# Kernel optimization log

Measured on AMD Instinct MI355X. Metric: run time of the kernel, lower is better.

The kernel has to match this reference:

```python
import jax, jax.numpy as jnp
import numpy as np

DELTA_T = 0.25
K_SUB = int(round(1.0 / DELTA_T))  # Euler substeps per observation (unit-spaced times)


def setup_inputs() -> dict:
    key = jax.random.key(0)
    ks = jax.random.split(key, 16)
    B, T, IN, XH, G, HID, OUT = 512, 128, 128, 512, 256, 256, 128
    s = 0.05
    inp = {
        "H": jax.random.normal(ks[0], (B, T, IN), jnp.float32),
        "times": jnp.arange(T, dtype=jnp.int64 if jax.config.jax_enable_x64 else jnp.int32).reshape(1, T),
        # x_model: Linear(IN,XH) -> ReLU -> Linear(XH,G); stored as [in,out]
        "W1": jax.random.normal(ks[1], (IN, XH), jnp.float32) * s,
        "b1": jax.random.normal(ks[2], (XH,), jnp.float32) * s,
        "W2": jax.random.normal(ks[3], (XH, G), jnp.float32) * s,
        "b2": jax.random.normal(ks[4], (G,), jnp.float32) * s,
        # FullGRUODECell_Autonomous: three bias-free [HID,HID] linears (torch [out,in])
        "Ohr": jax.random.normal(ks[5], (HID, HID), jnp.float32) * s,
        "Ohz": jax.random.normal(ks[6], (HID, HID), jnp.float32) * s,
        "Ohh": jax.random.normal(ks[7], (HID, HID), jnp.float32) * s,
        # torch.nn.GRU(G, HID): weights [3H, in], gate order r,z,n
        "Wih": jax.random.normal(ks[8], (3 * HID, G), jnp.float32) * s,
        "Whh": jax.random.normal(ks[9], (3 * HID, HID), jnp.float32) * s,
        "bih": jax.random.normal(ks[10], (3 * HID,), jnp.float32) * s,
        "bhh": jax.random.normal(ks[11], (3 * HID,), jnp.float32) * s,
        # rec_linear: Linear(G, OUT), stored as [in,out]
        "Wr": jax.random.normal(ks[12], (G, OUT), jnp.float32) * s,
        "br": jax.random.normal(ks[13], (OUT,), jnp.float32) * s,
    }
    return inp


def _forward(H, W1, b1, W2, b2, Ohr, Ohz, Ohh, Wih, Whh, bih, bhh, Wr, br):
    # x_model
    HH = jnp.maximum(H @ W1 + b1, 0.0) @ W2 + b2  # [B, T, G]
    B = HH.shape[0]
    HID = Ohr.shape[0]

    # GRU-ODE Euler substep (autonomous cell: input is implicitly zero)
    def ode_substep(h, _):
        r = jax.nn.sigmoid(h @ Ohr.T)
        z = jax.nn.sigmoid(h @ Ohz.T)
        u = jnp.tanh((r * h) @ Ohh.T)
        return h + DELTA_T * ((1.0 - z) * (u - h)), None

    Wir, Wiz, Win = jnp.split(Wih, 3, axis=0)
    Uhr, Uhz, Uhn = jnp.split(Whh, 3, axis=0)
    bir, biz, bin_ = jnp.split(bih, 3)
    bhr, bhz, bhn = jnp.split(bhh, 3)

    def step(h, x_t):  # x_t: [B, G]
        h, _ = jax.lax.scan(ode_substep, h, None, length=K_SUB)
        r = jax.nn.sigmoid(x_t @ Wir.T + bir + h @ Uhr.T + bhr)
        z = jax.nn.sigmoid(x_t @ Wiz.T + biz + h @ Uhz.T + bhz)
        n = jnp.tanh(x_t @ Win.T + bin_ + r * (h @ Uhn.T + bhn))
        h_new = (1.0 - z) * n + z * h  # GRU output for one step == new hidden
        return h_new, h_new

    h0 = jnp.zeros((B, HID), HH.dtype)
    _, outs = jax.lax.scan(step, h0, jnp.swapaxes(HH, 0, 1))  # [T, B, HID]
    out = jnp.swapaxes(outs, 0, 1)  # [B, T, HID] (== gru_input_size)
    return out @ Wr + br  # identity last activation


def reference(H, times, W1, b1, W2, b2, Ohr, Ohz, Ohh, Wih, Whh, bih, bhh, Wr, br):
    # times are unit-spaced (arange); the data-dependent while-loop of the
    # original reduces to exactly K_SUB Euler substeps before each observation.
    return _forward(H, W1, b1, W2, b2, Ohr, Ohz, Ohh, Wih, Whh, bih, bhh, Wr, br)
```

## Files before the change

### kernel.cpp

```cpp
#include <hip/hip_runtime.h>

typedef unsigned short ushort;
typedef unsigned int uint;
typedef __bf16 bf16x8 __attribute__((ext_vector_type(8)));
typedef ushort ushort8 __attribute__((ext_vector_type(8)));
typedef float f32x4 __attribute__((ext_vector_type(4)));

#define Z4 f32x4{0.f, 0.f, 0.f, 0.f}

__device__ __forceinline__ f32x4 mfma16(bf16x8 a, bf16x8 b, f32x4 c) {
    return __builtin_amdgcn_mfma_f32_16x16x32_bf16(a, b, c, 0, 0, 0);
}
__device__ __forceinline__ float bf2f(ushort h) {
    union { uint u; float f; } v; v.u = ((uint)h) << 16; return v.f;
}
__device__ __forceinline__ ushort f2bf(float f) {
    union { float f; uint u; } v; v.f = f;
    uint u = v.u;
    uint r = (u + 0x7fffu + ((u >> 16) & 1u)) >> 16;
    return (ushort)r;
}
__device__ __forceinline__ float sigmoidf_(float x) { return 1.f / (1.f + __expf(-x)); }
__device__ __forceinline__ float tanhf_(float x) {
    float e = __expf(2.f * x);
    return 1.f - 2.f / (e + 1.f);
}

typedef __attribute__((address_space(1))) uint guint;
typedef __attribute__((address_space(3))) uint luint;
__device__ __forceinline__ void dma16(const ushort* g, ushort* l) {
    __builtin_amdgcn_global_load_lds((const guint*)g, (luint*)l, 16, 0, 0);
}
template <int N> __device__ __forceinline__ void ring_wait() {
    asm volatile("s_waitcnt vmcnt(%0)" ::"n"(N) : "memory");
}
__device__ __forceinline__ void wg_sync() {
    asm volatile("s_waitcnt lgkmcnt(0)\n\ts_barrier" ::: "memory");
}

__global__ void pack_direct_k(const float* __restrict__ src, ushort* __restrict__ dst,
                              int N, int K) {
    int total = (N >> 4) * (K >> 5) * 64;
    int idx = blockIdx.x * 256 + threadIdx.x;
    if (idx >= total) return;
    int l = idx & 63, f = idx >> 6;
    int kfrags = K >> 5;
    int nt = f / kfrags, kf = f - nt * kfrags;
    int n = nt * 16 + (l & 15);
    int k0 = kf * 32 + (l >> 4) * 8;
    const float* s = src + (size_t)n * K + k0;
    ushort8 u;
#pragma unroll
    for (int j = 0; j < 8; j++) u[j] = f2bf(s[j]);
    *(ushort8*)&dst[(size_t)f * 512 + l * 8] = u;
}
__global__ void pack_trans_k(const float* __restrict__ src, ushort* __restrict__ dst,
                             int N, int K) {
    int total = (N >> 4) * (K >> 5) * 64;
    int idx = blockIdx.x * 256 + threadIdx.x;
    if (idx >= total) return;
    int l = idx & 63, f = idx >> 6;
    int kfrags = K >> 5;
    int nt = f / kfrags, kf = f - nt * kfrags;
    int n = nt * 16 + (l & 15);
    int k0 = kf * 32 + (l >> 4) * 8;
    ushort8 u;
#pragma unroll
    for (int j = 0; j < 8; j++) u[j] = f2bf(src[(size_t)(k0 + j) * N + n]);
    *(ushort8*)&dst[(size_t)f * 512 + l * 8] = u;
}

__global__ __launch_bounds__(256) void mlp_kernel(
    const float* __restrict__ H,
    const ushort* __restrict__ W1P,
    const float* __restrict__ b1,
    const ushort* __restrict__ W2P,
    const float* __restrict__ b2,
    ushort* __restrict__ X2)
{
    __shared__ __align__(16) ushort sH[64][136];
    __shared__ __align__(16) ushort sT[64][264];
    __shared__ float sb1[512], sb2[256];
    const int tid = threadIdx.x;
    const int w = tid >> 6, lane = tid & 63;
    const int q = lane >> 4, tc = lane & 15;
    const int lo8 = lane * 8;
    const int m0 = blockIdx.x * 64;

    {
        int r = tid >> 2, c0 = (tid & 3) * 32;
        const float* src = H + (size_t)(m0 + r) * 128 + c0;
#pragma unroll
        for (int v = 0; v < 4; v++) {
            float4 a = *(const float4*)(src + v * 8);
            float4 b = *(const float4*)(src + v * 8 + 4);
            ushort8 u;
            u[0] = f2bf(a.x); u[1] = f2bf(a.y); u[2] = f2bf(a.z); u[3] = f2bf(a.w);
            u[4] = f2bf(b.x); u[5] = f2bf(b.y); u[6] = f2bf(b.z); u[7] = f2bf(b.w);
            *(ushort8*)&sH[r][c0 + v * 8] = u;
        }
    }
    for (int i = tid; i < 512; i += 256) sb1[i] = b1[i];
    if (tid < 256) sb2[tid] = b2[tid];
    __syncthreads();

    bf16x8 af[4];
#pragma unroll
    for (int kb = 0; kb < 4; kb++) af[kb] = *(const bf16x8*)&sH[w * 16 + tc][kb * 32 + q * 8];

    f32x4 accH[16];
#pragma unroll
    for (int nt = 0; nt < 16; nt++) accH[nt] = Z4;

#pragma unroll 1
    for (int half = 0; half < 2; half++) {
        __syncthreads();
#pragma unroll
        for (int j = 0; j < 16; j++) {
            int n = half * 256 + j * 16 + tc;
            const ushort* bp = W1P + (size_t)((half * 16 + j) * 4) * 512 + lo8;
            f32x4 a = Z4;
#pragma unroll
            for (int kb = 0; kb < 4; kb++)
                a = mfma16(af[kb], *(const bf16x8*)(bp + kb * 512), a);
            float bv = sb1[n];
#pragma unroll
            for (int i = 0; i < 4; i++)
                sT[w * 16 + q * 4 + i][j * 16 + tc] = f2bf(fmaxf(a[i] + bv, 0.f));
        }
        __syncthreads();

        bf16x8 a2[8];
#pragma unroll
        for (int kb = 0; kb < 8; kb++) a2[kb] = *(const bf16x8*)&sT[w * 16 + tc][kb * 32 + q * 8];
#pragma unroll
        for (int nt = 0; nt < 16; nt++) {
            const ushort* bp = W2P + (size_t)(nt * 16 + half * 8) * 512 + lo8;
#pragma unroll
            for (int kb = 0; kb < 8; kb++)
                accH[nt] = mfma16(a2[kb], *(const bf16x8*)(bp + kb * 512), accH[nt]);
        }
    }

#pragma unroll
    for (int nt = 0; nt < 16; nt++) {
        int col = nt * 16 + tc;
        float bv = sb2[col];
#pragma unroll
        for (int i = 0; i < 4; i++)
            X2[(size_t)(m0 + w * 16 + q * 4 + i) * 256 + col] = f2bf(accH[nt][i] + bv);
    }
}

__global__ __launch_bounds__(256) void gemm128P(
    const ushort* __restrict__ A, const ushort* __restrict__ BP,
    const float* __restrict__ bias, void* __restrict__ Cout,
    int M, int N, int K, int mode)
{
    __shared__ __align__(16) ushort sA[128][40];
    const int tid = threadIdx.x;
    const int lane = tid & 63, wid = tid >> 6;
    const int q = lane >> 4, tc = lane & 15;
    const int lo8 = lane * 8;
    const int wm = (wid >> 1) * 64, wn = (wid & 1) * 64;
    const int bm = blockIdx.y * 128, bn = blockIdx.x * 128;

    f32x4 acc[4][4];
#pragma unroll
    for (int im = 0; im < 4; im++)
#pragma unroll
        for (int in_ = 0; in_ < 4; in_++) acc[im][in_] = Z4;

    const int arow = tid >> 1, acol = (tid & 1) * 16;
    const int kfrags = K >> 5;

    for (int kc = 0; kc < K; kc += 32) {
        const ushort* ga = A + (size_t)(bm + arow) * K + kc + acol;
        ushort8 va0 = *(const ushort8*)ga;
        ushort8 va1 = *(const ushort8*)(ga + 8);
        __syncthreads();
        *(ushort8*)&sA[arow][acol] = va0;
        *(ushort8*)&sA[arow][acol + 8] = va1;
        __syncthreads();

        bf16x8 af[4], bf[4];
#pragma unroll
        for (int im = 0; im < 4; im++) af[im] = *(const bf16x8*)&sA[wm + im * 16 + tc][q * 8];
#pragma unroll
        for (int in_ = 0; in_ < 4; in_++) {
            int nt = ((bn + wn) >> 4) + in_;
            bf[in_] = *(const bf16x8*)(BP + (size_t)(nt * kfrags + (kc >> 5)) * 512 + lo8);
        }
#pragma unroll
        for (int im = 0; im < 4; im++)
#pragma unroll
            for (int in_ = 0; in_ < 4; in_++)
                acc[im][in_] = mfma16(af[im], bf[in_], acc[im][in_]);
    }

#pragma unroll
    for (int in_ = 0; in_ < 4; in_++) {
        int col = bn + wn + in_ * 16 + tc;
        float bv = bias[col];
#pragma unroll
        for (int im = 0; im < 4; im++) {
            int row0 = bm + wm + im * 16 + q * 4;
#pragma unroll
            for (int r = 0; r < 4; r++) {
                float v = acc[im][in_][r] + bv;
                int row = row0 + r;
                if (mode == 0) {
                    ((ushort*)Cout)[(size_t)row * N + col] = f2bf(v);
                } else if (mode == 1) {
                    ((float*)Cout)[(size_t)row * N + col] = v;
                } else {
                    int b = row >> 7, t = row & 127;
                    size_t dst = (((size_t)(b >> 4) * 128 + t) * N + col) * 16 + (b & 15);
                    ((ushort*)Cout)[dst] = f2bf(v);
                }
            }
        }
    }
}

__global__ __launch_bounds__(1024) void scan_fused(
    const ushort* __restrict__ XgSw,
    const ushort* __restrict__ OhrP, const ushort* __restrict__ OhzP,
    const ushort* __restrict__ OhhP,
    const ushort* __restrict__ WhhP,
    const float*  __restrict__ bhh,
    ushort* __restrict__ hseq)
{
    const int bx = blockIdx.x;
    const int m0 = bx * 8;
    const int tid = threadIdx.x;
    const int w = tid >> 6, lane = tid & 63;
    const int q = lane >> 4, tc = lane & 15;
    const int lo8 = lane * 8;
    const int colbase = w * 16 + tc;
    const int R = ((lane >> 4) & 1) * 4 + ((lane >> 5) << 1);
    const bool lo = (q < 2);

    __shared__ __align__(16) ushort ring[16][3][1024];
    __shared__ __align__(16) ushort h_bf[16][264];
    __shared__ __align__(16) ushort rh_bf[16][264];

    for (int i = tid; i < 16 * 264; i += 1024) (&h_bf[0][0])[i] = 0;
    for (int i = tid; i < 16 * 264; i += 1024) (&rh_bf[0][0])[i] = 0;

    float rbv = bhh[colbase], zbv = bhh[256 + colbase], hnbv = bhh[512 + colbase];

    bf16x8 wOr[8], wOz[8];
#pragma unroll
    for (int f = 0; f < 8; f++) {
        wOr[f] = *(const bf16x8*)(OhrP + (size_t)(w * 8 + f) * 512 + lo8);
        wOz[f] = *(const bf16x8*)(OhzP + (size_t)(w * 8 + f) * 512 + lo8);
    }

    float hreg[2] = {0.f, 0.f};

    int ic = 0, islot = 0, slot = 0;
    auto pump = [&]() {
        if (ic >= 28) return;
        asm volatile("s_waitcnt lgkmcnt(0)" ::: "memory");
        const ushort* g;
        if (ic < 16) {
            g = OhhP + (size_t)(w * 8 + (ic & 3) * 2) * 512;
        } else {
            int j = ic - 16, gg = j % 3, kc = j / 3;
            g = WhhP + (size_t)((gg * 16 + w) * 8 + kc * 2) * 512;
        }
        g += lo8;
        ushort* sb = &ring[w][islot][0];
        dma16(g, sb); dma16(g + 512, sb + 512);
        ic++; islot = (islot == 2) ? 0 : islot + 1;
    };

    __syncthreads();

#pragma unroll 1
    for (int t = 0; t < 128; t++) {
        const ushort* xgp = XgSw + (((size_t)(bx >> 1) * 128 + t) * 768) * 16
                            + (bx & 1) * 8 + R;
        uint xg[3];
#pragma unroll
        for (int g = 0; g < 3; g++)
            xg[g] = *(const uint*)(xgp + (size_t)(g * 256 + colbase) * 16);

        ic = 0; islot = 0; slot = 0;
        pump(); pump(); pump();

#pragma unroll 1
        for (int s = 0; s < 4; s++) {
            f32x4 ar = Z4, az = Z4;
#pragma unroll
            for (int kh = 0; kh < 2; kh++) {
                bf16x8 af[4];
#pragma unroll
                for (int k = 0; k < 4; k++)
                    af[k] = *(const bf16x8*)&h_bf[tc][(kh * 4 + k) * 32 + q * 8];
#pragma unroll
                for (int k = 0; k < 4; k++) {
                    ar = mfma16(af[k], wOr[kh * 4 + k], ar);
                    az = mfma16(af[k], wOz[kh * 4 + k], az);
                }
            }
            float ar2 = __shfl(ar[2], lane & 31), ar3 = __shfl(ar[3], lane & 31);
            float az2 = __shfl(az[2], lane & 31), az3 = __shfl(az[3], lane & 31);
            float ea0 = lo ? ar[0] : ar2, ea1 = lo ? ar[1] : ar3;
            float ez0 = lo ? az[0] : az2, ez1 = lo ? az[1] : az3;
            rh_bf[R + 0][colbase] = f2bf(sigmoidf_(ea0) * hreg[0]);
            rh_bf[R + 1][colbase] = f2bf(sigmoidf_(ea1) * hreg[1]);
            wg_sync();

            f32x4 uu = Z4;
#pragma unroll
            for (int cc = 0; cc < 4; cc++) {
                bf16x8 au0 = *(const bf16x8*)&rh_bf[tc][(cc * 2) * 32 + q * 8];
                bf16x8 au1 = *(const bf16x8*)&rh_bf[tc][(cc * 2 + 1) * 32 + q * 8];
                ring_wait<4>();
                const ushort* sb = &ring[w][slot][0] + lo8;
                bf16x8 v0 = *(const bf16x8*)(sb);
                bf16x8 v1 = *(const bf16x8*)(sb + 512);
                slot = (slot == 2) ? 0 : slot + 1;
                pump();
                uu = mfma16(au0, v0, uu);
                uu = mfma16(au1, v1, uu);
            }
            float uu2 = __shfl(uu[2], lane & 31), uu3 = __shfl(uu[3], lane & 31);
            float eu0 = lo ? uu[0] : uu2, eu1 = lo ? uu[1] : uu3;
            {
                float zv = sigmoidf_(ez0), hv = hreg[0];
                float hn = hv + 0.25f * (1.f - zv) * (tanhf_(eu0) - hv);
                hreg[0] = hn;
                h_bf[R + 0][colbase] = f2bf(hn);
            }
            {
                float zv = sigmoidf_(ez1), hv = hreg[1];
                float hn = hv + 0.25f * (1.f - zv) * (tanhf_(eu1) - hv);
                hreg[1] = hn;
                h_bf[R + 1][colbase] = f2bf(hn);
            }
            wg_sync();
        }

        f32x4 accr = Z4, accz = Z4, accn = Z4;
#define GRU_CHUNK(J, WN)                                                       \
        {                                                                      \
            constexpr int g_ = (J) % 3, kc_ = (J) / 3;                         \
            bf16x8 ah0 = *(const bf16x8*)&h_bf[tc][(kc_ * 2) * 32 + q * 8];    \
            bf16x8 ah1 = *(const bf16x8*)&h_bf[tc][(kc_ * 2 + 1) * 32 + q * 8];\
            ring_wait<WN>();                                                   \
            const ushort* sb = &ring[w][slot][0] + lo8;                        \
            bf16x8 v0 = *(const bf16x8*)(sb);                                  \
            bf16x8 v1 = *(const bf16x8*)(sb + 512);                            \
            slot = (slot == 2) ? 0 : slot + 1;                                 \
            pump();                                                            \
            f32x4* tg = (g_ == 0) ? &accr : (g_ == 1) ? &accz : &accn;         \
            *tg = mfma16(ah0, v0, *tg);                                        \
            *tg = mfma16(ah1, v1, *tg);                                        \
        }
        GRU_CHUNK(0, 4)  GRU_CHUNK(1, 4)  GRU_CHUNK(2, 4)  GRU_CHUNK(3, 4)
        GRU_CHUNK(4, 4)  GRU_CHUNK(5, 4)  GRU_CHUNK(6, 4)  GRU_CHUNK(7, 4)
        GRU_CHUNK(8, 4)  GRU_CHUNK(9, 4)  GRU_CHUNK(10, 2) GRU_CHUNK(11, 0)
#undef GRU_CHUNK
        wg_sync();

        {
            float r2 = __shfl(accr[2], lane & 31), r3 = __shfl(accr[3], lane & 31);
            float z2 = __shfl(accz[2], lane & 31), z3 = __shfl(accz[3], lane & 31);
            float n2 = __shfl(accn[2], lane & 31), n3 = __shfl(accn[3], lane & 31);
            float er0 = lo ? accr[0] : r2, er1 = lo ? accr[1] : r3;
            float ez0 = lo ? accz[0] : z2, ez1 = lo ? accz[1] : z3;
            float en0 = lo ? accn[0] : n2, en1 = lo ? accn[1] : n3;
            {
                float xr = bf2f((ushort)(xg[0])), xz = bf2f((ushort)(xg[1])),
                      xn = bf2f((ushort)(xg[2]));
                float rg = sigmoidf_(er0 + xr + rbv);
                float zg = sigmoidf_(ez0 + xz + zbv);
                float ng = tanhf_(xn + rg * (en0 + hnbv));
                float hv = hreg[0];
                float hn = (1.f - zg) * ng + zg * hv;
                hreg[0] = hn;
                h_bf[R + 0][colbase] = f2bf(hn);
            }
            {
                float xr = bf2f((ushort)(xg[0] >> 16)), xz = bf2f((ushort)(xg[1] >> 16)),
                      xn = bf2f((ushort)(xg[2] >> 16));
                float rg = sigmoidf_(er1 + xr + rbv);
                float zg = sigmoidf_(ez1 + xz + zbv);
                float ng = tanhf_(xn + rg * (en1 + hnbv));
                float hv = hreg[1];
                float hn = (1.f - zg) * ng + zg * hv;
                hreg[1] = hn;
                h_bf[R + 1][colbase] = f2bf(hn);
            }
        }
        wg_sync();

        {
            int row = tid >> 7, col = (tid & 127) * 2;
            *(uint*)&hseq[((size_t)(m0 + row) * 128 + t) * 256 + col] =
                *(const uint*)&h_bf[row][col];
        }
    }
}

extern "C" void kernel_launch(void* const* d_in, const int* in_sizes, int n_in,
                              void* d_out, int out_size, void* d_ws, size_t ws_size,
                              hipStream_t stream) {
    const float* H   = (const float*)d_in[0];
    const float* W1  = (const float*)d_in[2];
    const float* b1  = (const float*)d_in[3];
    const float* W2  = (const float*)d_in[4];
    const float* b2  = (const float*)d_in[5];
    const float* Ohr = (const float*)d_in[6];
    const float* Ohz = (const float*)d_in[7];
    const float* Ohh = (const float*)d_in[8];
    const float* Wih = (const float*)d_in[9];
    const float* Whh = (const float*)d_in[10];
    const float* bih = (const float*)d_in[11];
    const float* bhh = (const float*)d_in[12];
    const float* Wr  = (const float*)d_in[13];
    const float* br  = (const float*)d_in[14];
    float* out = (float*)d_out;
    char* ws = (char*)d_ws;

    ushort* Xg   = (ushort*)(ws);
    ushort* X2   = (ushort*)(ws + 100663296);
    ushort* hseq = X2;
    char* pk = ws + 134217728;
    ushort* W1P  = (ushort*)(pk);
    ushort* W2P  = (ushort*)(pk + 131072);
    ushort* WrP  = (ushort*)(pk + 393216);
    ushort* OhrP = (ushort*)(pk + 458752);
    ushort* OhzP = (ushort*)(pk + 589824);
    ushort* OhhP = (ushort*)(pk + 720896);
    ushort* WihP = (ushort*)(pk + 851968);

    pack_trans_k<<<dim3(32),  256, 0, stream>>>(W1,  W1P, 512, 128);
    pack_trans_k<<<dim3(64),  256, 0, stream>>>(W2,  W2P, 256, 512);
    pack_trans_k<<<dim3(16),  256, 0, stream>>>(Wr,  WrP, 128, 256);
    pack_direct_k<<<dim3(32), 256, 0, stream>>>(Ohr, OhrP, 256, 256);
    pack_direct_k<<<dim3(32), 256, 0, stream>>>(Ohz, OhzP, 256, 256);
    pack_direct_k<<<dim3(32), 256, 0, stream>>>(Ohh, OhhP, 256, 256);
    pack_direct_k<<<dim3(96), 256, 0, stream>>>(Wih, WihP, 768, 256);
    pack_direct_k<<<dim3(96), 256, 0, stream>>>(Whh, (ushort*)(pk + 1245184), 768, 256);
    ushort* WhhP = (ushort*)(pk + 1245184);

    mlp_kernel<<<dim3(1024), 256, 0, stream>>>(H, W1P, b1, W2P, b2, X2);
    gemm128P<<<dim3(6, 512), 256, 0, stream>>>(X2, WihP, bih, Xg, 65536, 768, 256, 2);

    scan_fused<<<dim3(64), 1024, 0, stream>>>(Xg, OhrP, OhzP, OhhP, WhhP, bhh, hseq);

    gemm128P<<<dim3(1, 512), 256, 0, stream>>>(hseq, WrP, br, out, 65536, 128, 256, 1);
}
```

Measured before the change: 2.520 ms.

## Swizzle hidden-state LDS layout and deepen weight ring to four slots

Removes the padded h_bf/rh_bf rows and applies an XOR swizzle on column addresses, keyed by row, to avoid LDS bank conflicts on the 16-byte fragment reads and scalar writes. It also grows the per-wave weight staging ring from three to four slots, reorders the Whh chunk sequence gate-major, and raises the outstanding-load waits so more DMA prefetches stay in flight. The cost is more shared memory, which may limit occupancy, and more complex indexing.

New measurement: 2.828 ms. 12.2% more time.

```diff
diff --git a/kernel.cpp b/kernel.cpp
--- a/kernel.cpp
+++ b/kernel.cpp
@@ -240,13 +240,16 @@
     const int colbase = w * 16 + tc;
     const int R = ((lane >> 4) & 1) * 4 + ((lane >> 5) << 1);
     const bool lo = (q < 2);
-
-    __shared__ __align__(16) ushort ring[16][3][1024];
-    __shared__ __align__(16) ushort h_bf[16][264];
-    __shared__ __align__(16) ushort rh_bf[16][264];
-
-    for (int i = tid; i < 16 * 264; i += 1024) (&h_bf[0][0])[i] = 0;
-    for (int i = tid; i < 16 * 264; i += 1024) (&rh_bf[0][0])[i] = 0;
+    const int rsw = (tc & 7) << 3;
+    const int wc0 = colbase ^ ((R & 7) << 3);
+    const int wc1 = colbase ^ (((R + 1) & 7) << 3);
+
+    __shared__ __align__(16) ushort ring[16][4][1024];
+    __shared__ __align__(16) ushort h_bf[16][256];
+    __shared__ __align__(16) ushort rh_bf[16][256];
+
+    for (int i = tid; i < 16 * 256; i += 1024) (&h_bf[0][0])[i] = 0;
+    for (int i = tid; i < 16 * 256; i += 1024) (&rh_bf[0][0])[i] = 0;
 
     float rbv = bhh[colbase], zbv = bhh[256 + colbase], hnbv = bhh[512 + colbase];
 
@@ -258,6 +261,9 @@
     }
 
     float hreg[2] = {0.f, 0.f};
+
+    const int srow = tid >> 7, scol = (tid & 127) * 2;
+    const ushort* s_src = &h_bf[srow][scol ^ ((srow & 7) << 3)];
 
     int ic = 0, islot = 0, slot = 0;
     auto pump = [&]() {
@@ -267,13 +273,13 @@
         if (ic < 16) {
             g = OhhP + (size_t)(w * 8 + (ic & 3) * 2) * 512;
         } else {
-            int j = ic - 16, gg = j % 3, kc = j / 3;
+            int j = ic - 16, gg = j >> 2, kc = j & 3;
             g = WhhP + (size_t)((gg * 16 + w) * 8 + kc * 2) * 512;
         }
         g += lo8;
         ushort* sb = &ring[w][islot][0];
         dma16(g, sb); dma16(g + 512, sb + 512);
-        ic++; islot = (islot == 2) ? 0 : islot + 1;
+        ic++; islot = (islot + 1) & 3;
     };
 
     __syncthreads();
@@ -288,7 +294,7 @@
             xg[g] = *(const uint*)(xgp + (size_t)(g * 256 + colbase) * 16);
 
         ic = 0; islot = 0; slot = 0;
-        pump(); pump(); pump();
+        pump(); pump(); pump(); pump();
 
 #pragma unroll 1
         for (int s = 0; s < 4; s++) {
@@ -298,7 +304,7 @@
                 bf16x8 af[4];
 #pragma unroll
                 for (int k = 0; k < 4; k++)
-                    af[k] = *(const bf16x8*)&h_bf[tc][(kh * 4 + k) * 32 + q * 8];
+                    af[k] = *(const bf16x8*)&h_bf[tc][((kh * 4 + k) * 32 + q * 8) ^ rsw];
 #pragma unroll
                 for (int k = 0; k < 4; k++) {
                     ar = mfma16(af[k], wOr[kh * 4 + k], ar);
@@ -309,20 +315,20 @@
             float az2 = __shfl(az[2], lane & 31), az3 = __shfl(az[3], lane & 31);
             float ea0 = lo ? ar[0] : ar2, ea1 = lo ? ar[1] : ar3;
             float ez0 = lo ? az[0] : az2, ez1 = lo ? az[1] : az3;
-            rh_bf[R + 0][colbase] = f2bf(sigmoidf_(ea0) * hreg[0]);
-            rh_bf[R + 1][colbase] = f2bf(sigmoidf_(ea1) * hreg[1]);
+            rh_bf[R + 0][wc0] = f2bf(sigmoidf_(ea0) * hreg[0]);
+            rh_bf[R + 1][wc1] = f2bf(sigmoidf_(ea1) * hreg[1]);
             wg_sync();
 
             f32x4 uu = Z4;
 #pragma unroll
             for (int cc = 0; cc < 4; cc++) {
-                bf16x8 au0 = *(const bf16x8*)&rh_bf[tc][(cc * 2) * 32 + q * 8];
-                bf16x8 au1 = *(const bf16x8*)&rh_bf[tc][(cc * 2 + 1) * 32 + q * 8];
-                ring_wait<4>();
+                bf16x8 au0 = *(const bf16x8*)&rh_bf[tc][((cc * 2) * 32 + q * 8) ^ rsw];
+                bf16x8 au1 = *(const bf16x8*)&rh_bf[tc][((cc * 2 + 1) * 32 + q * 8) ^ rsw];
+                ring_wait<6>();
                 const ushort* sb = &ring[w][slot][0] + lo8;
                 bf16x8 v0 = *(const bf16x8*)(sb);
                 bf16x8 v1 = *(const bf16x8*)(sb + 512);
-                slot = (slot == 2) ? 0 : slot + 1;
+                slot = (slot + 1) & 3;
                 pump();
                 uu = mfma16(au0, v0, uu);
                 uu = mfma16(au1, v1, uu);
@@ -333,13 +339,13 @@
                 float zv = sigmoidf_(ez0), hv = hreg[0];
                 float hn = hv + 0.25f * (1.f - zv) * (tanhf_(eu0) - hv);
                 hreg[0] = hn;
-                h_bf[R + 0][colbase] = f2bf(hn);
+                h_bf[R + 0][wc0] = f2bf(hn);
             }
             {
                 float zv = sigmoidf_(ez1), hv = hreg[1];
                 float hn = hv + 0.25f * (1.f - zv) * (tanhf_(eu1) - hv);
                 hreg[1] = hn;
-                h_bf[R + 1][colbase] = f2bf(hn);
+                h_bf[R + 1][wc1] = f2bf(hn);
             }
             wg_sync();
         }
@@ -347,22 +353,22 @@
         f32x4 accr = Z4, accz = Z4, accn = Z4;
 #define GRU_CHUNK(J, WN)                                                       \
         {                                                                      \
-            constexpr int g_ = (J) % 3, kc_ = (J) / 3;                         \
-            bf16x8 ah0 = *(const bf16x8*)&h_bf[tc][(kc_ * 2) * 32 + q * 8];    \
-            bf16x8 ah1 = *(const bf16x8*)&h_bf[tc][(kc_ * 2 + 1) * 32 + q * 8];\
+            constexpr int g_ = (J) >> 2, kc_ = (J) & 3;                        \
+            bf16x8 ah0 = *(const bf16x8*)&h_bf[tc][((kc_ * 2) * 32 + q * 8) ^ rsw];     \
+            bf16x8 ah1 = *(const bf16x8*)&h_bf[tc][((kc_ * 2 + 1) * 32 + q * 8) ^ rsw]; \
             ring_wait<WN>();                                                   \
             const ushort* sb = &ring[w][slot][0] + lo8;                        \
             bf16x8 v0 = *(const bf16x8*)(sb);                                  \
             bf16x8 v1 = *(const bf16x8*)(sb + 512);                            \
-            slot = (slot == 2) ? 0 : slot + 1;                                 \
+            slot = (slot + 1) & 3;                                             \
             pump();                                                            \
             f32x4* tg = (g_ == 0) ? &accr : (g_ == 1) ? &accz : &accn;         \
             *tg = mfma16(ah0, v0, *tg);                                        \
             *tg = mfma16(ah1, v1, *tg);                                        \
         }
-        GRU_CHUNK(0, 4)  GRU_CHUNK(1, 4)  GRU_CHUNK(2, 4)  GRU_CHUNK(3, 4)
-        GRU_CHUNK(4, 4)  GRU_CHUNK(5, 4)  GRU_CHUNK(6, 4)  GRU_CHUNK(7, 4)
-        GRU_CHUNK(8, 4)  GRU_CHUNK(9, 4)  GRU_CHUNK(10, 2) GRU_CHUNK(11, 0)
+        GRU_CHUNK(0, 6)  GRU_CHUNK(1, 6)  GRU_CHUNK(2, 6)  GRU_CHUNK(3, 6)
+        GRU_CHUNK(4, 6)  GRU_CHUNK(5, 6)  GRU_CHUNK(6, 6)  GRU_CHUNK(7, 6)
+        GRU_CHUNK(8, 6)  GRU_CHUNK(9, 4)  GRU_CHUNK(10, 2) GRU_CHUNK(11, 0)
 #undef GRU_CHUNK
         wg_sync();
 
@@ -382,7 +388,7 @@
                 float hv = hreg[0];
                 float hn = (1.f - zg) * ng + zg * hv;
                 hreg[0] = hn;
-                h_bf[R + 0][colbase] = f2bf(hn);
+                h_bf[R + 0][wc0] = f2bf(hn);
             }
             {
                 float xr = bf2f((ushort)(xg[0] >> 16)), xz = bf2f((ushort)(xg[1] >> 16)),
@@ -393,16 +399,13 @@
                 float hv = hreg[1];
                 float hn = (1.f - zg) * ng + zg * hv;
                 hreg[1] = hn;
-                h_bf[R + 1][colbase] = f2bf(hn);
+                h_bf[R + 1][wc1] = f2bf(hn);
             }
         }
         wg_sync();
 
-        {
-            int row = tid >> 7, col = (tid & 127) * 2;
-            *(uint*)&hseq[((size_t)(m0 + row) * 128 + t) * 256 + col] =
-                *(const uint*)&h_bf[row][col];
-        }
+        *(uint*)&hseq[((size_t)(m0 + srow) * 128 + t) * 256 + scol] =
+            *(const uint*)s_src;
     }
 }
 
```
